# Optimization experiments

Hardware: AMD Instinct MI355X
Metric: run time of the kernel (lower is better)

The kernel has to match this reference:

```python
import jax, jax.numpy as jnp
import numpy as np

D_MODEL = 768

def setup_inputs() -> dict:
    key = jax.random.key(0)
    k1, k2, k3, k4 = jax.random.split(key, 4)
    x = jax.random.normal(k1, (2, 2048, D_MODEL), dtype=jnp.float32)
    w_qkv = jax.random.normal(k2, (3 * D_MODEL, D_MODEL), dtype=jnp.float32) * (1.0 / np.sqrt(D_MODEL))
    w_fc = jax.random.normal(k3, (D_MODEL, D_MODEL), dtype=jnp.float32) * (1.0 / np.sqrt(D_MODEL))
    b_fc = jax.random.normal(k4, (D_MODEL,), dtype=jnp.float32) * 0.01
    return {"x": x, "w_qkv": w_qkv, "w_fc": w_fc, "b_fc": b_fc, "n_head": 12}


def reference(x, w_qkv, w_fc, b_fc, n_head):
    b, n, d = x.shape
    h = int(n_head)
    d_k = d // h
    temperature = float(d_k) ** 0.5  # NOTE: source MULTIPLIES by sqrt(d_k)
    qkv = x @ w_qkv.T                                  # [b, n, 3d] (qkv_bias=False)
    # rearrange 'b n (qkv d h) -> qkv b h n d' : split order is (qkv, d_k, h)
    qkv = qkv.reshape(b, n, 3, d_k, h).transpose(2, 0, 4, 1, 3)  # [3, b, h, n, d_k]
    q, k, v = qkv[0], qkv[1], qkv[2]
    attn = jnp.einsum('bhid,bhjd->bhij', q, k) * temperature      # [b, h, n, n]
    attn = jax.nn.softmax(attn, axis=-1)                           # dropout p=0 -> identity
    out = jnp.einsum('bhij,bhjd->bhid', attn, v)                   # [b, h, n, d_k]
    out = out.transpose(0, 2, 1, 3).reshape(b, n, d)               # 'b h n d -> b n (h d)'
    out = out @ w_fc.T + b_fc                                      # fc (dropout p=0 -> identity)
    return out
```

## Files before the change

kernel.cpp:

```cpp
#include <hip/hip_runtime.h>
#include <stdint.h>

typedef float f32x4 __attribute__((ext_vector_type(4)));
typedef _Float16 f16;
typedef f16 f16x8 __attribute__((ext_vector_type(8)));
typedef f16 f16x4 __attribute__((ext_vector_type(4)));

#define MFMA16(a, b, c) __builtin_amdgcn_mfma_f32_16x16x32_f16((a), (b), (c), 0, 0, 0)

typedef __attribute__((address_space(1))) const uint32_t gu32;
typedef __attribute__((address_space(3))) uint32_t lu32;
__device__ __forceinline__ void gload_lds16(const void* g, void* l) {
    __builtin_amdgcn_global_load_lds((gu32*)g, (lu32*)l, 16, 0, 0);
}

__device__ __forceinline__ size_t kv_elem(int bh, int n, int d) {
    const int kt = n >> 6, row = n & 63;
    return ((size_t)(bh * 32 + kt)) * 4096 + row * 64 + (((d >> 3) ^ (row & 7)) << 3) + (d & 7);
}

__global__ void split_inputs(const float* __restrict__ X, const float* __restrict__ Wq,
                             const float* __restrict__ Wf,
                             f16* __restrict__ Xh, f16* __restrict__ Xl,
                             f16* __restrict__ Wh, f16* __restrict__ Wfb) {
    const int tid = blockIdx.x * 256 + threadIdx.x;
    if (tid < 393216) {
        const float* s = X + (size_t)tid * 8;
        f16 hi[8], lo[8];
#pragma unroll
        for (int j = 0; j < 8; j += 4) {
            f32x4 v = *(const f32x4*)(s + j);
#pragma unroll
            for (int q = 0; q < 4; ++q) {
                f16 h = (f16)v[q];
                hi[j + q] = h;
                lo[j + q] = (f16)(v[q] - (float)h);
            }
        }
        *(f16x8*)(Xh + (size_t)tid * 8) = *(f16x8*)hi;
        *(f16x8*)(Xl + (size_t)tid * 8) = *(f16x8*)lo;
    } else if (tid < 614400) {
        const int t2 = tid - 393216;
        const int row = t2 / 96;
        const int k = (t2 % 96) * 8;
        const int c = row / 768;
        const int rem = row - c * 768;
        const int d = rem / 12;
        const int h2 = rem - d * 12;
        const int cp = c * 768 + h2 * 64 + d;
        const float* s = Wq + (size_t)row * 768 + k;
        f16 hi[8];
#pragma unroll
        for (int j = 0; j < 8; j += 4) {
            f32x4 v = *(const f32x4*)(s + j);
#pragma unroll
            for (int q = 0; q < 4; ++q) hi[j + q] = (f16)v[q];
        }
        *(f16x8*)(Wh + (size_t)cp * 768 + k) = *(f16x8*)hi;
    } else {
        const int t2 = tid - 614400;
        const float* s = Wf + (size_t)t2 * 8;
        f16 hi[8];
#pragma unroll
        for (int j = 0; j < 8; j += 4) {
            f32x4 v = *(const f32x4*)(s + j);
#pragma unroll
            for (int q = 0; q < 4; ++q) hi[j + q] = (f16)v[q];
        }
        *(f16x8*)(Wfb + (size_t)t2 * 8) = *(f16x8*)hi;
    }
}

__global__ __launch_bounds__(256) void qkv_gemm(
    const f16* __restrict__ Xh, const f16* __restrict__ Xl,
    const f16* __restrict__ Wh,
    f16* __restrict__ Qh, f16* __restrict__ Ql,
    f16* __restrict__ Khg, f16* __restrict__ Vb) {
    __shared__ f16 Ah[128 * 32], Al[128 * 32], Bh[128 * 32];
    const int t = threadIdx.x;
    const int lane = t & 63, wv = t >> 6;
    const int wm = (wv >> 1) * 64, wn = (wv & 1) * 64;
    const int r = lane & 15, g = lane >> 4;
    const int bm = blockIdx.x, bn = blockIdx.y;
    const bool full = (bn < 12);

    const int lrow = lane >> 2;
    const int lk = (lane & 3) * 8;

    f32x4 acc[4][4];
#pragma unroll
    for (int i = 0; i < 4; ++i)
#pragma unroll
        for (int j = 0; j < 4; ++j) acc[i][j] = (f32x4)0.0f;

    for (int ks = 0; ks < 768; ks += 32) {
#pragma unroll
        for (int hh = 0; hh < 2; ++hh) {
            const int ii = wv * 2 + hh;
            const int grow = ii * 16 + lrow;
            const size_t ga = (size_t)(bm * 128 + grow) * 768 + ks + lk;
            const size_t gb = (size_t)(bn * 128 + grow) * 768 + ks + lk;
            const int lbase = ii * 512;
            gload_lds16(Xh + ga, &Ah[lbase]);
            gload_lds16(Wh + gb, &Bh[lbase]);
            if (full) gload_lds16(Xl + ga, &Al[lbase]);
        }
        __syncthreads();

        f16x8 a_h[4], b[4];
#pragma unroll
        for (int mf = 0; mf < 4; ++mf) a_h[mf] = *(f16x8*)&Ah[(wm + mf * 16 + r) * 32 + g * 8];
#pragma unroll
        for (int nf = 0; nf < 4; ++nf) b[nf] = *(f16x8*)&Bh[(wn + nf * 16 + r) * 32 + g * 8];
        if (full) {
            f16x8 a_l[4];
#pragma unroll
            for (int mf = 0; mf < 4; ++mf) a_l[mf] = *(f16x8*)&Al[(wm + mf * 16 + r) * 32 + g * 8];
#pragma unroll
            for (int mf = 0; mf < 4; ++mf)
#pragma unroll
                for (int nf = 0; nf < 4; ++nf) {
                    acc[mf][nf] = MFMA16(a_h[mf], b[nf], acc[mf][nf]);
                    acc[mf][nf] = MFMA16(a_l[mf], b[nf], acc[mf][nf]);
                }
        } else {
#pragma unroll
            for (int mf = 0; mf < 4; ++mf)
#pragma unroll
                for (int nf = 0; nf < 4; ++nf)
                    acc[mf][nf] = MFMA16(a_h[mf], b[nf], acc[mf][nf]);
        }
        __syncthreads();
    }

    const int comp = bn / 6;
#pragma unroll
    for (int mf = 0; mf < 4; ++mf)
#pragma unroll
        for (int nf = 0; nf < 4; ++nf) {
            const int col = bn * 128 + wn + nf * 16 + r;
            const int h = (col >> 6) % 12;
            const int d = col & 63;
#pragma unroll
            for (int v = 0; v < 4; ++v) {
                const int row = bm * 128 + wm + mf * 16 + g * 4 + v;
                const int b2 = row >> 11, n = row & 2047;
                const int bh = b2 * 12 + h;
                float val = acc[mf][nf][v];
                if (comp == 0) {
                    const size_t dest = ((size_t)bh * 2048 + n) * 64 + d;
                    val *= 8.0f;
                    f16 hi = (f16)val;
                    Qh[dest] = hi;
                    Ql[dest] = (f16)(val - (float)hi);
                } else if (comp == 1) {
                    Khg[kv_elem(bh, n, d)] = (f16)val;
                } else {
                    Vb[((size_t)bh * 2048 + n) * 64 + d] = (f16)val;
                }
            }
        }
}

__global__ void v_transpose(const f16* __restrict__ Vb, f16* __restrict__ VTg) {
    __shared__ f16 Vt[64 * 72];
    const int t = threadIdx.x;
    const int tile = blockIdx.x;
    const f16* src = Vb + (size_t)tile * 4096;
    const int row = t >> 2, d0 = (t & 3) * 16;
    *(f16x8*)&Vt[row * 72 + d0]     = *(const f16x8*)(src + row * 64 + d0);
    *(f16x8*)&Vt[row * 72 + d0 + 8] = *(const f16x8*)(src + row * 64 + d0 + 8);
    __syncthreads();
    f16* dst = VTg + (size_t)tile * 4096;
#pragma unroll
    for (int it = 0; it < 2; ++it) {
        const int c = t + it * 256;
        const int kc = c >> 8;
        const int d = (c >> 2) & 63;
        const int gg = c & 3;
        const int gl = gg ^ ((d >> 1) & 3);
        f16 o[8];
#pragma unroll
        for (int j = 0; j < 8; ++j) {
            const int kv = kc * 32 + (j >> 2) * 16 + gl * 4 + (j & 3);
            o[j] = Vt[kv * 72 + d];
        }
        *(f16x8*)(dst + (size_t)c * 8) = *(f16x8*)o;
    }
}

__global__ __launch_bounds__(256) void attn_partial(
    const f16* __restrict__ Qh, const f16* __restrict__ Ql,
    const f16* __restrict__ Khg, const f16* __restrict__ VTg,
    f16* __restrict__ OP, float* __restrict__ Mst, float* __restrict__ Lst) {
    __shared__ f16 Khs[4096], VTs[4096];

    const int t = threadIdx.x;
    const int lane = t & 63, wv = t >> 6;
    const int r = lane & 15, g = lane >> 4;
    const int bid = blockIdx.x;
    const int qb = bid & 15;
    const int half = (bid >> 4) & 1;
    const int bh = bid >> 5;
    const size_t headoff = (size_t)bh * 2048 * 64;
    const int q0w = qb * 128 + wv * 32;

    f16x8 qh[2][2], ql[2][2];
#pragma unroll
    for (int qf = 0; qf < 2; ++qf)
#pragma unroll
        for (int kc = 0; kc < 2; ++kc) {
            const size_t off = headoff + (size_t)(q0w + qf * 16 + r) * 64 + kc * 32 + g * 8;
            qh[qf][kc] = *(const f16x8*)(Qh + off);
            ql[qf][kc] = *(const f16x8*)(Ql + off);
        }

    f32x4 o_accT[2][4];
    float m_run[2] = {-1e30f, -1e30f}, l_run[2] = {0.0f, 0.0f};
#pragma unroll
    for (int qf = 0; qf < 2; ++qf)
#pragma unroll
        for (int df = 0; df < 4; ++df) o_accT[qf][df] = (f32x4)0.0f;

    for (int kt = half * 16; kt < half * 16 + 16; ++kt) {
        const size_t tb = ((size_t)bh * 32 + kt) * 4096;
#pragma unroll
        for (int c2 = 0; c2 < 2; ++c2) {
            const int c = wv * 2 + c2;
            const int go = c * 512 + lane * 8;
            gload_lds16(Khg + tb + go, &Khs[c * 512]);
            gload_lds16(VTg + tb + go, &VTs[c * 512]);
        }
        __syncthreads();

        f32x4 s[2][4];
#pragma unroll
        for (int qf = 0; qf < 2; ++qf)
#pragma unroll
            for (int cf = 0; cf < 4; ++cf) s[qf][cf] = (f32x4)0.0f;
#pragma unroll
        for (int kc = 0; kc < 2; ++kc) {
            f16x8 ka[4];
#pragma unroll
            for (int cf = 0; cf < 4; ++cf)
                ka[cf] = *(f16x8*)&Khs[(cf * 16 + r) * 64 + (((kc * 4 + g) ^ (r & 7)) << 3)];
#pragma unroll
            for (int cf = 0; cf < 4; ++cf)
#pragma unroll
                for (int qf = 0; qf < 2; ++qf) {
                    s[qf][cf] = MFMA16(ka[cf], qh[qf][kc], s[qf][cf]);
                    s[qf][cf] = MFMA16(ka[cf], ql[qf][kc], s[qf][cf]);
                }
        }

        f16x8 pa[2][2];
#pragma unroll
        for (int qf = 0; qf < 2; ++qf) {
            float mx = -1e30f;
#pragma unroll
            for (int cf = 0; cf < 4; ++cf)
#pragma unroll
                for (int v = 0; v < 4; ++v) mx = fmaxf(mx, s[qf][cf][v]);
            mx = fmaxf(mx, __shfl_xor(mx, 16));
            mx = fmaxf(mx, __shfl_xor(mx, 32));
            const float mn = fmaxf(m_run[qf], mx);
            const float sc = __expf(m_run[qf] - mn);
            m_run[qf] = mn;
            float rs = 0.0f;
#pragma unroll
            for (int cf = 0; cf < 4; ++cf)
#pragma unroll
                for (int v = 0; v < 4; ++v) {
                    const float p = __expf(s[qf][cf][v] - mn);
                    rs += p;
                    pa[qf][cf >> 1][(cf & 1) * 4 + v] = (f16)p;
                }
            rs += __shfl_xor(rs, 16);
            rs += __shfl_xor(rs, 32);
            l_run[qf] = l_run[qf] * sc + rs;
#pragma unroll
            for (int df = 0; df < 4; ++df) o_accT[qf][df] *= sc;
        }

#pragma unroll
        for (int kc = 0; kc < 2; ++kc)
#pragma unroll
            for (int df = 0; df < 4; ++df) {
                f16x8 vb = *(f16x8*)&VTs[kc * 2048 + (df * 16 + r) * 32 +
                                         ((g ^ ((r >> 1) & 3)) << 3)];
#pragma unroll
                for (int qf = 0; qf < 2; ++qf)
                    o_accT[qf][df] = MFMA16(vb, pa[qf][kc], o_accT[qf][df]);
            }
        __syncthreads();
    }

    const int pb = (bh << 1) + half;
#pragma unroll
    for (int qf = 0; qf < 2; ++qf) {
        const int n = q0w + qf * 16 + r;
        if (g == 0) {
            Mst[pb * 2048 + n] = m_run[qf];
            Lst[pb * 2048 + n] = l_run[qf];
        }
#pragma unroll
        for (int df = 0; df < 4; ++df) {
            f16 o4[4];
#pragma unroll
            for (int v = 0; v < 4; ++v) o4[v] = (f16)o_accT[qf][df][v];
            *(f16x4*)&OP[((size_t)pb * 2048 + n) * 64 + df * 16 + g * 4] = *(f16x4*)o4;
        }
    }
}

__global__ void attn_combine(const f16* __restrict__ OP, const float* __restrict__ Mst,
                             const float* __restrict__ Lst, f16* __restrict__ AO) {
    const int tid = blockIdx.x * 256 + threadIdx.x;
    const int d4 = (tid & 15) * 4;
    const int pr = tid >> 4;
    const int bh = pr >> 11, n = pr & 2047;
    const int i1 = (bh * 2) * 2048 + n, i2 = i1 + 2048;
    const float m1 = Mst[i1], m2 = Mst[i2];
    const float l1 = Lst[i1], l2 = Lst[i2];
    const float m = fmaxf(m1, m2);
    const float w1 = __expf(m1 - m), w2 = __expf(m2 - m);
    const float inv = 1.0f / (w1 * l1 + w2 * l2);
    f16x4 o1 = *(const f16x4*)(OP + (size_t)i1 * 64 + d4);
    f16x4 o2 = *(const f16x4*)(OP + (size_t)i2 * 64 + d4);
    const int b = bh / 12, h = bh - b * 12;
    f16 out[4];
#pragma unroll
    for (int j = 0; j < 4; ++j)
        out[j] = (f16)((w1 * (float)o1[j] + w2 * (float)o2[j]) * inv);
    *(f16x4*)(AO + ((size_t)(b * 2048 + n)) * 768 + h * 64 + d4) = *(f16x4*)out;
}

__global__ __launch_bounds__(256) void fc_gemm(const f16* __restrict__ A,
                                               const f16* __restrict__ Wfb,
                                               const float* __restrict__ bias,
                                               float* __restrict__ OUT) {
    __shared__ f16 As[64 * 64], Bs[64 * 64];
    const int t = threadIdx.x;
    const int lane = t & 63, wv = t >> 6;
    const int wm = (wv >> 1) * 32, wn = (wv & 1) * 32;
    const int r = lane & 15, g = lane >> 4;
    const int bm = blockIdx.x, bn = blockIdx.y;

    f32x4 acc[2][2];
#pragma unroll
    for (int i = 0; i < 2; ++i)
#pragma unroll
        for (int j = 0; j < 2; ++j) acc[i][j] = (f32x4)0.0f;

    const int srow = t >> 2;
    const int ssg = (t & 3) * 2;

    for (int ks = 0; ks < 768; ks += 64) {
        const f16* as = A + (size_t)(bm * 64 + srow) * 768 + ks;
        const f16* bs = Wfb + (size_t)(bn * 64 + srow) * 768 + ks;
#pragma unroll
        for (int u = 0; u < 2; ++u) {
            const int sg = ssg + u;
            const int dst = srow * 64 + ((sg ^ (srow & 7)) << 3);
            *(f16x8*)&As[dst] = *(const f16x8*)(as + sg * 8);
            *(f16x8*)&Bs[dst] = *(const f16x8*)(bs + sg * 8);
        }
        __syncthreads();

#pragma unroll
        for (int kc = 0; kc < 2; ++kc) {
            f16x8 a[2], b[2];
#pragma unroll
            for (int mf = 0; mf < 2; ++mf) {
                const int row = wm + mf * 16 + r;
                a[mf] = *(f16x8*)&As[row * 64 + (((kc * 4 + g) ^ (row & 7)) << 3)];
            }
#pragma unroll
            for (int nf = 0; nf < 2; ++nf) {
                const int row = wn + nf * 16 + r;
                b[nf] = *(f16x8*)&Bs[row * 64 + (((kc * 4 + g) ^ (row & 7)) << 3)];
            }
#pragma unroll
            for (int mf = 0; mf < 2; ++mf)
#pragma unroll
                for (int nf = 0; nf < 2; ++nf)
                    acc[mf][nf] = MFMA16(a[mf], b[nf], acc[mf][nf]);
        }
        __syncthreads();
    }

#pragma unroll
    for (int nf = 0; nf < 2; ++nf) {
        const int col = bn * 64 + wn + nf * 16 + r;
        const float bv = bias[col];
#pragma unroll
        for (int mf = 0; mf < 2; ++mf) {
            const int row = bm * 64 + wm + mf * 16 + g * 4;
#pragma unroll
            for (int v = 0; v < 4; ++v)
                OUT[(size_t)(row + v) * 768 + col] = acc[mf][nf][v] + bv;
        }
    }
}

extern "C" void kernel_launch(void* const* d_in, const int* in_sizes, int n_in,
                              void* d_out, int out_size, void* d_ws, size_t ws_size,
                              hipStream_t stream) {
    (void)in_sizes; (void)n_in; (void)out_size; (void)ws_size;
    const float* x     = (const float*)d_in[0];
    const float* w_qkv = (const float*)d_in[1];
    const float* w_fc  = (const float*)d_in[2];
    const float* b_fc  = (const float*)d_in[3];
    float* out = (float*)d_out;

    char* ws = (char*)d_ws;
    f16* Xh  = (f16*)ws;
    f16* Xl  = Xh + 3145728;
    f16* Qh  = Xl + 3145728;
    f16* Ql  = Qh + 3145728;
    f16* Khg = Ql + 3145728;
    f16* Vb  = Khg + 3145728;
    f16* VTg = Vb + 3145728;
    f16* AO  = VTg + 3145728;
    f16* Wh  = AO + 3145728;
    f16* Wfb = Wh + 1769472;
    float* Mst = (float*)(Wfb + 589824);
    float* Lst = Mst + 98304;
    f16* OP  = (f16*)(Lst + 98304);

    split_inputs<<<2688, 256, 0, stream>>>(x, w_qkv, w_fc, Xh, Xl, Wh, Wfb);
    qkv_gemm<<<dim3(32, 18), 256, 0, stream>>>(Xh, Xl, Wh, Qh, Ql, Khg, Vb);
    v_transpose<<<768, 256, 0, stream>>>(Vb, VTg);
    attn_partial<<<768, 256, 0, stream>>>(Qh, Ql, Khg, VTg, OP, Mst, Lst);
    attn_combine<<<3072, 256, 0, stream>>>(OP, Mst, Lst, AO);
    fc_gemm<<<dim3(64, 12), 256, 0, stream>>>(AO, Wfb, b_fc, out);
}
```

Baseline: 145.3 us.

## Double-buffer LDS in QKV GEMM and attention; split keys three ways

Both the QKV GEMM and the attention partial kernel now use double-buffered shared memory. The next tile is prefetched asynchronously while the current one is computed, which removes one barrier per iteration. The attention kernel also splits the key range into three parts (11/11/10 tiles) instead of two, giving 1152 blocks for better occupancy across CUs. The combine kernel is updated to merge three partials. This costs more LDS per block and more partial-result traffic in exchange for more parallelism and load/compute overlap.

```diff
diff --git a/kernel.cpp b/kernel.cpp
--- a/kernel.cpp
+++ b/kernel.cpp
@@ -76,7 +76,7 @@
     const f16* __restrict__ Wh,
     f16* __restrict__ Qh, f16* __restrict__ Ql,
     f16* __restrict__ Khg, f16* __restrict__ Vb) {
-    __shared__ f16 Ah[128 * 32], Al[128 * 32], Bh[128 * 32];
+    __shared__ f16 Ah[2][4096], Al[2][4096], Bh[2][4096];
     const int t = threadIdx.x;
     const int lane = t & 63, wv = t >> 6;
     const int wm = (wv >> 1) * 64, wn = (wv & 1) * 64;
@@ -93,29 +93,34 @@
 #pragma unroll
         for (int j = 0; j < 4; ++j) acc[i][j] = (f32x4)0.0f;
 
-    for (int ks = 0; ks < 768; ks += 32) {
+    auto stage = [&](int ksi, int buf) {
 #pragma unroll
         for (int hh = 0; hh < 2; ++hh) {
             const int ii = wv * 2 + hh;
             const int grow = ii * 16 + lrow;
-            const size_t ga = (size_t)(bm * 128 + grow) * 768 + ks + lk;
-            const size_t gb = (size_t)(bn * 128 + grow) * 768 + ks + lk;
-            const int lbase = ii * 512;
-            gload_lds16(Xh + ga, &Ah[lbase]);
-            gload_lds16(Wh + gb, &Bh[lbase]);
-            if (full) gload_lds16(Xl + ga, &Al[lbase]);
-        }
+            const size_t ga = (size_t)(bm * 128 + grow) * 768 + ksi * 32 + lk;
+            const size_t gb = (size_t)(bn * 128 + grow) * 768 + ksi * 32 + lk;
+            gload_lds16(Xh + ga, &Ah[buf][ii * 512]);
+            gload_lds16(Wh + gb, &Bh[buf][ii * 512]);
+            if (full) gload_lds16(Xl + ga, &Al[buf][ii * 512]);
+        }
+    };
+
+    stage(0, 0);
+    int cur = 0;
+    for (int i = 0; i < 24; ++i) {
         __syncthreads();
+        if (i < 23) stage(i + 1, cur ^ 1);
 
         f16x8 a_h[4], b[4];
 #pragma unroll
-        for (int mf = 0; mf < 4; ++mf) a_h[mf] = *(f16x8*)&Ah[(wm + mf * 16 + r) * 32 + g * 8];
-#pragma unroll
-        for (int nf = 0; nf < 4; ++nf) b[nf] = *(f16x8*)&Bh[(wn + nf * 16 + r) * 32 + g * 8];
+        for (int mf = 0; mf < 4; ++mf) a_h[mf] = *(f16x8*)&Ah[cur][(wm + mf * 16 + r) * 32 + g * 8];
+#pragma unroll
+        for (int nf = 0; nf < 4; ++nf) b[nf] = *(f16x8*)&Bh[cur][(wn + nf * 16 + r) * 32 + g * 8];
         if (full) {
             f16x8 a_l[4];
 #pragma unroll
-            for (int mf = 0; mf < 4; ++mf) a_l[mf] = *(f16x8*)&Al[(wm + mf * 16 + r) * 32 + g * 8];
+            for (int mf = 0; mf < 4; ++mf) a_l[mf] = *(f16x8*)&Al[cur][(wm + mf * 16 + r) * 32 + g * 8];
 #pragma unroll
             for (int mf = 0; mf < 4; ++mf)
 #pragma unroll
@@ -130,7 +135,7 @@
                 for (int nf = 0; nf < 4; ++nf)
                     acc[mf][nf] = MFMA16(a_h[mf], b[nf], acc[mf][nf]);
         }
-        __syncthreads();
+        cur ^= 1;
     }
 
     const int comp = bn / 6;
@@ -193,17 +198,20 @@
     const f16* __restrict__ Qh, const f16* __restrict__ Ql,
     const f16* __restrict__ Khg, const f16* __restrict__ VTg,
     f16* __restrict__ OP, float* __restrict__ Mst, float* __restrict__ Lst) {
-    __shared__ f16 Khs[4096], VTs[4096];
+    __shared__ f16 Khs[2][4096], VTs[2][4096];
 
     const int t = threadIdx.x;
     const int lane = t & 63, wv = t >> 6;
     const int r = lane & 15, g = lane >> 4;
     const int bid = blockIdx.x;
     const int qb = bid & 15;
-    const int half = (bid >> 4) & 1;
-    const int bh = bid >> 5;
+    const int pb = bid >> 4;
+    const int part = pb % 3;
+    const int bh = pb / 3;
     const size_t headoff = (size_t)bh * 2048 * 64;
     const int q0w = qb * 128 + wv * 32;
+    const int kt0 = part * 11;
+    const int nt = (part == 2) ? 10 : 11;
 
     f16x8 qh[2][2], ql[2][2];
 #pragma unroll
@@ -222,16 +230,22 @@
 #pragma unroll
         for (int df = 0; df < 4; ++df) o_accT[qf][df] = (f32x4)0.0f;
 
-    for (int kt = half * 16; kt < half * 16 + 16; ++kt) {
+    auto stage = [&](int kt, int buf) {
         const size_t tb = ((size_t)bh * 32 + kt) * 4096;
 #pragma unroll
         for (int c2 = 0; c2 < 2; ++c2) {
             const int c = wv * 2 + c2;
             const int go = c * 512 + lane * 8;
-            gload_lds16(Khg + tb + go, &Khs[c * 512]);
-            gload_lds16(VTg + tb + go, &VTs[c * 512]);
-        }
+            gload_lds16(Khg + tb + go, &Khs[buf][c * 512]);
+            gload_lds16(VTg + tb + go, &VTs[buf][c * 512]);
+        }
+    };
+
+    stage(kt0, 0);
+    int cur = 0;
+    for (int i = 0; i < nt; ++i) {
         __syncthreads();
+        if (i + 1 < nt) stage(kt0 + i + 1, cur ^ 1);
 
         f32x4 s[2][4];
 #pragma unroll
@@ -243,7 +257,7 @@
             f16x8 ka[4];
 #pragma unroll
             for (int cf = 0; cf < 4; ++cf)
-                ka[cf] = *(f16x8*)&Khs[(cf * 16 + r) * 64 + (((kc * 4 + g) ^ (r & 7)) << 3)];
+                ka[cf] = *(f16x8*)&Khs[cur][(cf * 16 + r) * 64 + (((kc * 4 + g) ^ (r & 7)) << 3)];
 #pragma unroll
             for (int cf = 0; cf < 4; ++cf)
 #pragma unroll
@@ -286,16 +300,15 @@
         for (int kc = 0; kc < 2; ++kc)
 #pragma unroll
             for (int df = 0; df < 4; ++df) {
-                f16x8 vb = *(f16x8*)&VTs[kc * 2048 + (df * 16 + r) * 32 +
-                                         ((g ^ ((r >> 1) & 3)) << 3)];
+                f16x8 vb = *(f16x8*)&VTs[cur][kc * 2048 + (df * 16 + r) * 32 +
+                                             ((g ^ ((r >> 1) & 3)) << 3)];
 #pragma unroll
                 for (int qf = 0; qf < 2; ++qf)
                     o_accT[qf][df] = MFMA16(vb, pa[qf][kc], o_accT[qf][df]);
             }
-        __syncthreads();
-    }
-
-    const int pb = (bh << 1) + half;
+        cur ^= 1;
+    }
+
 #pragma unroll
     for (int qf = 0; qf < 2; ++qf) {
         const int n = q0w + qf * 16 + r;
@@ -319,19 +332,19 @@
     const int d4 = (tid & 15) * 4;
     const int pr = tid >> 4;
     const int bh = pr >> 11, n = pr & 2047;
-    const int i1 = (bh * 2) * 2048 + n, i2 = i1 + 2048;
-    const float m1 = Mst[i1], m2 = Mst[i2];
-    const float l1 = Lst[i1], l2 = Lst[i2];
-    const float m = fmaxf(m1, m2);
-    const float w1 = __expf(m1 - m), w2 = __expf(m2 - m);
-    const float inv = 1.0f / (w1 * l1 + w2 * l2);
-    f16x4 o1 = *(const f16x4*)(OP + (size_t)i1 * 64 + d4);
-    f16x4 o2 = *(const f16x4*)(OP + (size_t)i2 * 64 + d4);
+    const int i0 = (bh * 3) * 2048 + n;
+    const float m0 = Mst[i0], m1 = Mst[i0 + 2048], m2 = Mst[i0 + 4096];
+    const float m = fmaxf(fmaxf(m0, m1), m2);
+    const float w0 = __expf(m0 - m), w1 = __expf(m1 - m), w2 = __expf(m2 - m);
+    const float inv = 1.0f / (w0 * Lst[i0] + w1 * Lst[i0 + 2048] + w2 * Lst[i0 + 4096]);
+    f16x4 o0 = *(const f16x4*)(OP + (size_t)i0 * 64 + d4);
+    f16x4 o1 = *(const f16x4*)(OP + (size_t)(i0 + 2048) * 64 + d4);
+    f16x4 o2 = *(const f16x4*)(OP + (size_t)(i0 + 4096) * 64 + d4);
     const int b = bh / 12, h = bh - b * 12;
     f16 out[4];
 #pragma unroll
     for (int j = 0; j < 4; ++j)
-        out[j] = (f16)((w1 * (float)o1[j] + w2 * (float)o2[j]) * inv);
+        out[j] = (f16)((w0 * (float)o0[j] + w1 * (float)o1[j] + w2 * (float)o2[j]) * inv);
     *(f16x4*)(AO + ((size_t)(b * 2048 + n)) * 768 + h * 64 + d4) = *(f16x4*)out;
 }
 
@@ -425,13 +438,13 @@
     f16* Wh  = AO + 3145728;
     f16* Wfb = Wh + 1769472;
     float* Mst = (float*)(Wfb + 589824);
-    float* Lst = Mst + 98304;
-    f16* OP  = (f16*)(Lst + 98304);
+    float* Lst = Mst + 147456;
+    f16* OP  = (f16*)(Lst + 147456);
 
     split_inputs<<<2688, 256, 0, stream>>>(x, w_qkv, w_fc, Xh, Xl, Wh, Wfb);
     qkv_gemm<<<dim3(32, 18), 256, 0, stream>>>(Xh, Xl, Wh, Qh, Ql, Khg, Vb);
     v_transpose<<<768, 256, 0, stream>>>(Vb, VTg);
-    attn_partial<<<768, 256, 0, stream>>>(Qh, Ql, Khg, VTg, OP, Mst, Lst);
+    attn_partial<<<1152, 256, 0, stream>>>(Qh, Ql, Khg, VTg, OP, Mst, Lst);
     attn_combine<<<3072, 256, 0, stream>>>(OP, Mst, Lst, AO);
     fc_gemm<<<dim3(64, 12), 256, 0, stream>>>(AO, Wfb, b_fc, out);
 }
```

After: 150.1 us. 1.03x slower.
